# Performance work log

Hardware: AMD Instinct MI355X
Metric: run time of the kernel (lower is better)

## Reference

```python
import jax, jax.numpy as jnp
import numpy as np

B, E, S, D = 32, 64, 50, 300   # batch, sentences/essay, words/sentence, word dim
F = 100                        # conv filters (cnn_lstm_convunits_size)
H = 100                        # lstm units (cnn_lstm_att_pool_size)
W_WIN = 5                      # word window length


def setup_inputs() -> dict:
    key = jax.random.key(0)
    ks = jax.random.split(key, 12)
    n = lambda k, shape: (jax.random.normal(k, shape, jnp.float32) * 0.05)
    return {
        "essays": jax.random.normal(ks[0], (B, E, S, D), jnp.float32),
        "conv_k": n(ks[1], (1, W_WIN, D, F)),      # HWIO
        "conv_b": jnp.zeros((F,), jnp.float32),
        "att1_mat": n(ks[2], (F, F)),
        "att1_bias": n(ks[3], (F,)),
        "att1_vec": n(ks[4], (F, 1)),
        "lstm_W": n(ks[5], (F + H, 4 * H)),        # TF BasicLSTMCell kernel, gate order i,j,f,o
        "lstm_b": jnp.zeros((4 * H,), jnp.float32),
        "att2_mat": n(ks[6], (H, H)),
        "att2_bias": n(ks[7], (H,)),
        "att2_vec": n(ks[8], (H, 1)),
        "dense_w": n(ks[9], (H, 1)),
        "dense_b": jnp.zeros((1,), jnp.float32),
    }


def reference(essays, conv_k, conv_b, att1_mat, att1_bias, att1_vec,
              lstm_W, lstm_b, att2_mat, att2_bias, att2_vec,
              dense_w, dense_b):
    # conv2d, kernel [1, w_window_len], SAME padding, relu  -> [B,E,S,F]
    conv1 = jax.lax.conv_general_dilated(
        essays, conv_k, window_strides=(1, 1), padding="SAME",
        dimension_numbers=("NHWC", "HWIO", "NHWC"))
    conv1 = jax.nn.relu(conv1 + conv_b)

    # attention pooling over words (axis=2)
    a1 = jnp.tanh(jnp.einsum("besf,fg->besg", conv1, att1_mat) + att1_bias)
    a1 = jnp.einsum("besg,go->beso", a1, att1_vec)          # [B,E,S,1]
    a1 = jax.nn.softmax(a1, axis=2)
    sent = jnp.sum(a1 * conv1, axis=2)                       # [B,E,F]

    # BasicLSTMCell (forget_bias=1.0, gate order i,j,f,o) over sentence axis
    hdim = lstm_b.shape[0] // 4
    bsz = essays.shape[0]

    def step(carry, xt):
        c, h = carry
        z = jnp.concatenate([xt, h], axis=1) @ lstm_W + lstm_b
        i, j, f, o = jnp.split(z, 4, axis=1)
        c = c * jax.nn.sigmoid(f + 1.0) + jax.nn.sigmoid(i) * jnp.tanh(j)
        h = jax.nn.sigmoid(o) * jnp.tanh(c)
        return (c, h), h

    init = (jnp.zeros((bsz, hdim), sent.dtype), jnp.zeros((bsz, hdim), sent.dtype))
    xs = jnp.swapaxes(sent, 0, 1)                            # [E,B,F]
    _, hs = jax.lax.scan(step, init, xs)
    lstm = jnp.swapaxes(hs, 0, 1)                            # [B,E,H]

    # attention pooling over sentences (axis=1)
    a2 = jnp.tanh(jnp.einsum("beh,hg->beg", lstm, att2_mat) + att2_bias)
    a2 = jnp.einsum("beg,go->beo", a2, att2_vec)             # [B,E,1]
    a2 = jax.nn.softmax(a2, axis=1)
    essay_repr = jnp.sum(a2 * lstm, axis=1)                  # [B,H]

    preds = jax.nn.sigmoid(essay_repr @ dense_w + dense_b).reshape(-1)  # [B]
    return preds
```

## Files before the change

### kernel.cpp

```cpp
#include <hip/hip_runtime.h>
#include <hip/hip_bf16.h>
#include <stdint.h>

#define Bsz 32
#define Esz 64
#define Ssz 50
#define Dsz 300
#define Fsz 100
#define Hsz 100
#define WWIN 5

#define PX   328
#define PC   136
#define KT_CONV 50
#define NTILES  7
#define MTILES  4
#define NGRP 2214

typedef __attribute__((ext_vector_type(8))) short bf16x8;
typedef __attribute__((ext_vector_type(8))) unsigned short u16x8;
typedef __attribute__((ext_vector_type(4))) float f32x4;

__device__ __forceinline__ float sigmoid_fast(float x) {
    return 1.0f / (1.0f + __expf(-x));
}
__device__ __forceinline__ float tanhf_fast(float x) {
    const float ax = fabsf(x);
    const float e = __expf(2.0f * ax);
    const float t = 1.0f - 2.0f / (e + 1.0f);
    return copysignf(t, x);
}

__device__ __forceinline__ unsigned short f2bf(float x) {
    union { __hip_bfloat16 h; unsigned short u; } cv;
    cv.h = __float2bfloat16(x);
    return cv.u;
}
__device__ __forceinline__ unsigned int f2bf2(float lo, float hi) {
    union { __hip_bfloat162 h2; unsigned int u; } cv;
    cv.h2 = __float22bfloat162_rn(make_float2(lo, hi));
    return cv.u;
}
__device__ __forceinline__ float bf2f(unsigned short b) {
    union { uint32_t u; float f; } v; v.u = ((uint32_t)b) << 16;
    return v.f;
}

#define N_BTGC (KT_CONV * 112 * 32)
#define N_BTGA (4 * 112 * 32)
#define N_BTGW (4 * 400 * 32)

__global__ __launch_bounds__(256) void prep_kernel(
    const float* __restrict__ conv_k, const float* __restrict__ att1_mat,
    const float* __restrict__ lstm_W,
    unsigned short* __restrict__ BtgC, unsigned short* __restrict__ BtgA,
    unsigned short* __restrict__ BtgW)
{
    const int total = N_BTGC + N_BTGA + N_BTGW;
    for (int i = blockIdx.x * 256 + threadIdx.x; i < total; i += gridDim.x * 256) {
        if (i < N_BTGC) {
            const int kt = i / (112 * 32);
            const int r  = i % (112 * 32);
            const int n  = r / 32;
            const int kk = r % 32;
            const int w  = kt / 10;
            const int d  = (kt % 10) * 32 + kk;
            float val = (d < Dsz && n < Fsz) ? conv_k[((size_t)w * Dsz + d) * Fsz + n] : 0.f;
            BtgC[i] = f2bf(val);
        } else if (i < N_BTGC + N_BTGA) {
            const int j  = i - N_BTGC;
            const int kt = j / (112 * 32);
            const int r  = j % (112 * 32);
            const int n  = r / 32;
            const int kk = r % 32;
            const int k  = kt * 32 + kk;
            float val = (k < Fsz && n < Fsz) ? att1_mat[(size_t)k * Fsz + n] : 0.f;
            BtgA[j] = f2bf(val);
        } else {
            const int j  = i - N_BTGC - N_BTGA;
            const int kt = j / (400 * 32);
            const int r  = j % (400 * 32);
            const int n  = r / 32;
            const int kk = r % 32;
            const int k  = kt * 32 + kk;
            float val = (k < Fsz) ? lstm_W[(size_t)k * 400 + n] : 0.f;
            BtgW[j] = f2bf(val);
        }
    }
}

template<int G>
__device__ __forceinline__ void conv_loadB(
    const unsigned short* __restrict__ BtgC, int boff0, int boff1, bool has1,
    bf16x8 (&bR)[5][2])
{
#pragma unroll
    for (int i = 0; i < 5; ++i) {
        const int kt = G * 5 + i;
        bR[i][0] = *reinterpret_cast<const bf16x8*>(BtgC + kt * 3584 + boff0);
        bR[i][1] = has1 ? *reinterpret_cast<const bf16x8*>(BtgC + kt * 3584 + boff1)
                        : (bf16x8)0;
    }
}

template<int KT>
__device__ __forceinline__ void conv_loadA(
    const unsigned short* b0p, const unsigned short* b1p,
    const int (&abase)[MTILES], bf16x8 (&a)[2][MTILES])
{
    constexpr int w   = KT / 10;
    constexpr int t   = KT % 10;
    constexpr int off = w * PX + t * 32;
#pragma unroll
    for (int mt = 0; mt < MTILES; ++mt) {
        a[0][mt] = *reinterpret_cast<const bf16x8*>(&b0p[abase[mt] + off]);
        a[1][mt] = *reinterpret_cast<const bf16x8*>(&b1p[abase[mt] + off]);
    }
}

__device__ __forceinline__ void mfma16(
    const bf16x8 (&a)[2][MTILES], const bf16x8 (&b)[2], bool has1,
    f32x4 (&acc)[2][MTILES][2])
{
    __builtin_amdgcn_s_setprio(1);
#pragma unroll
    for (int es = 0; es < 2; ++es) {
#pragma unroll
        for (int mt = 0; mt < MTILES; ++mt) {
            acc[es][mt][0] = __builtin_amdgcn_mfma_f32_16x16x32_bf16(a[es][mt], b[0], acc[es][mt][0], 0, 0, 0);
            if (has1)
                acc[es][mt][1] = __builtin_amdgcn_mfma_f32_16x16x32_bf16(a[es][mt], b[1], acc[es][mt][1], 0, 0, 0);
        }
    }
    __builtin_amdgcn_s_setprio(0);
}

template<int KT>
__device__ __forceinline__ void conv_kt(
    const unsigned short* b0p, const unsigned short* b1p,
    const int (&abase)[MTILES], bool has1, const bf16x8 (&b)[2],
    bf16x8 (&aX)[2][MTILES], bf16x8 (&aY)[2][MTILES],
    f32x4 (&acc)[2][MTILES][2])
{
    constexpr bool even = (KT % 2) == 0;
    if constexpr (KT + 1 < KT_CONV) {
        if constexpr (even) conv_loadA<KT + 1>(b0p, b1p, abase, aY);
        else                conv_loadA<KT + 1>(b0p, b1p, abase, aX);
    }
    if constexpr (even) mfma16(aX, b, has1, acc);
    else                mfma16(aY, b, has1, acc);
}

template<int G>
__device__ __forceinline__ void conv_group(
    const unsigned short* b0p, const unsigned short* b1p,
    const int (&abase)[MTILES], bool has1, const bf16x8 (&bR)[5][2],
    bf16x8 (&aX)[2][MTILES], bf16x8 (&aY)[2][MTILES],
    f32x4 (&acc)[2][MTILES][2])
{
    conv_kt<G * 5 + 0>(b0p, b1p, abase, has1, bR[0], aX, aY, acc);
    conv_kt<G * 5 + 1>(b0p, b1p, abase, has1, bR[1], aX, aY, acc);
    conv_kt<G * 5 + 2>(b0p, b1p, abase, has1, bR[2], aX, aY, acc);
    conv_kt<G * 5 + 3>(b0p, b1p, abase, has1, bR[3], aX, aY, acc);
    conv_kt<G * 5 + 4>(b0p, b1p, abase, has1, bR[4], aX, aY, acc);
}

template<int KT>
__device__ __forceinline__ void att_loadA(
    const unsigned short* b0p, const unsigned short* b1p,
    const int (&abase2)[MTILES], bf16x8 (&a)[2][MTILES])
{
    constexpr int off = KT * 32;
#pragma unroll
    for (int mt = 0; mt < MTILES; ++mt) {
        a[0][mt] = *reinterpret_cast<const bf16x8*>(&b0p[abase2[mt] + off]);
        a[1][mt] = *reinterpret_cast<const bf16x8*>(&b1p[abase2[mt] + off]);
    }
}

__global__ __launch_bounds__(256, 2) void conv_att1_kernel(
    const float* __restrict__ essays,
    const unsigned short* __restrict__ BtgC,
    const unsigned short* __restrict__ BtgA,
    const float* __restrict__ conv_b,
    const float* __restrict__ att1_bias,
    const float* __restrict__ att1_vec,
    unsigned short* __restrict__ sent_bf)
{
    __shared__ __align__(16) unsigned short buf[2][54 * PX];
    __shared__ float u_s[2][64];
    __shared__ float alpha_s[2][64];

    const int be0 = blockIdx.x * 2;
    const int tid = threadIdx.x;
    const int lane = tid & 63;
    const int wid  = tid >> 6;
    const int ln   = lane & 15;
    const int qd   = lane >> 4;

    if (tid < 128) u_s[tid >> 6][tid & 63] = 0.f;

    const int nt0 = wid;
    const int nt1 = wid + 4;
    const bool has1 = (nt1 < NTILES);
    const int boff0 = (nt0 * 16 + ln) * 32 + 8 * qd;
    const int boff1 = (nt1 * 16 + ln) * 32 + 8 * qd;

    int abase[MTILES];
#pragma unroll
    for (int mt = 0; mt < MTILES; ++mt) {
        const int m = mt * 16 + ln;
        abase[mt] = (m < Ssz ? m : Ssz - 1) * PX + 8 * qd;
    }

    bf16x8 bX[5][2], bY[5][2];
    conv_loadB<0>(BtgC, boff0, boff1, has1, bX);
    conv_loadB<1>(BtgC, boff0, boff1, has1, bY);

#pragma unroll
    for (int es = 0; es < 2; ++es) {
        const float* in_g = essays + (size_t)(be0 + es) * (Ssz * Dsz);
        float4 va[9], vb[9];
        int rr[9], cc[9];
        bool hv[9], fv[9], gv[9];
#pragma unroll
        for (int it = 0; it < 9; ++it) {
            const int g  = tid + it * 256;
            const int r  = g / 41;
            const int c8 = (g - r * 41) * 8;
            const int s  = r - 2;
            gv[it] = (g < NGRP);
            hv[it] = gv[it] && (s >= 0) && (s < Ssz) && (c8 < Dsz);
            fv[it] = hv[it] && (c8 + 8 <= Dsz);
            const float* base = in_g + (hv[it] ? (s * Dsz + c8) : 0);
            va[it] = *reinterpret_cast<const float4*>(base);
            vb[it] = *reinterpret_cast<const float4*>(fv[it] ? base + 4 : base);
            rr[it] = r; cc[it] = c8;
        }
#pragma unroll
        for (int it = 0; it < 9; ++it) {
            if (!gv[it]) continue;
            const float e0 = hv[it] ? va[it].x : 0.f;
            const float e1 = hv[it] ? va[it].y : 0.f;
            const float e2 = hv[it] ? va[it].z : 0.f;
            const float e3 = hv[it] ? va[it].w : 0.f;
            const float e4 = fv[it] ? vb[it].x : 0.f;
            const float e5 = fv[it] ? vb[it].y : 0.f;
            const float e6 = fv[it] ? vb[it].z : 0.f;
            const float e7 = fv[it] ? vb[it].w : 0.f;
            uint4 o;
            o.x = f2bf2(e0, e1);
            o.y = f2bf2(e2, e3);
            o.z = f2bf2(e4, e5);
            o.w = f2bf2(e6, e7);
            *reinterpret_cast<uint4*>(&buf[es][rr[it] * PX + cc[it]]) = o;
        }
    }
    __syncthreads();

    const unsigned short* b0p = buf[0];
    const unsigned short* b1p = buf[1];

    f32x4 acc[2][MTILES][2];
#pragma unroll
    for (int es = 0; es < 2; ++es)
#pragma unroll
        for (int mt = 0; mt < MTILES; ++mt) { acc[es][mt][0] = (f32x4)0.f; acc[es][mt][1] = (f32x4)0.f; }

    {
        bf16x8 aX[2][MTILES], aY[2][MTILES];
        conv_loadA<0>(b0p, b1p, abase, aX);
        conv_group<0>(b0p, b1p, abase, has1, bX, aX, aY, acc);
        conv_loadB<2>(BtgC, boff0, boff1, has1, bX);
        conv_group<1>(b0p, b1p, abase, has1, bY, aX, aY, acc);
        conv_loadB<3>(BtgC, boff0, boff1, has1, bY);
        conv_group<2>(b0p, b1p, abase, has1, bX, aX, aY, acc);
        conv_loadB<4>(BtgC, boff0, boff1, has1, bX);
        conv_group<3>(b0p, b1p, abase, has1, bY, aX, aY, acc);
        conv_loadB<5>(BtgC, boff0, boff1, has1, bY);
        conv_group<4>(b0p, b1p, abase, has1, bX, aX, aY, acc);
        conv_loadB<6>(BtgC, boff0, boff1, has1, bX);
        conv_group<5>(b0p, b1p, abase, has1, bY, aX, aY, acc);
        conv_loadB<7>(BtgC, boff0, boff1, has1, bY);
        conv_group<6>(b0p, b1p, abase, has1, bX, aX, aY, acc);
        conv_loadB<8>(BtgC, boff0, boff1, has1, bX);
        conv_group<7>(b0p, b1p, abase, has1, bY, aX, aY, acc);
        conv_loadB<9>(BtgC, boff0, boff1, has1, bY);
        conv_group<8>(b0p, b1p, abase, has1, bX, aX, aY, acc);
        conv_group<9>(b0p, b1p, abase, has1, bY, aX, aY, acc);
    }

    bf16x8 a1b[4][2];
#pragma unroll
    for (int kt = 0; kt < 4; ++kt) {
        a1b[kt][0] = *reinterpret_cast<const bf16x8*>(BtgA + kt * 3584 + boff0);
        a1b[kt][1] = has1 ? *reinterpret_cast<const bf16x8*>(BtgA + kt * 3584 + boff1)
                          : (bf16x8)0;
    }
    __syncthreads();

    {
        const float bias0 = conv_b[nt0 * 16 + ln];
        const int n_g1 = nt1 * 16 + ln;
        const bool g1ok = has1 && (n_g1 < Fsz);
        const float bias1 = g1ok ? conv_b[n_g1] : 0.f;
#pragma unroll
        for (int es = 0; es < 2; ++es) {
#pragma unroll
            for (int mt = 0; mt < MTILES; ++mt) {
#pragma unroll
                for (int j = 0; j < 4; ++j) {
                    const int m_row = mt * 16 + qd * 4 + j;
                    buf[es][m_row * PC + nt0 * 16 + ln] = f2bf(fmaxf(acc[es][mt][0][j] + bias0, 0.f));
                    if (g1ok)
                        buf[es][m_row * PC + n_g1] = f2bf(fmaxf(acc[es][mt][1][j] + bias1, 0.f));
                }
            }
        }
    }
    for (int idx = tid; idx < 2 * 64 * 2; idx += 256) {
        const int es = idx >> 7;
        const int r2 = idx & 127;
        const int row = r2 >> 1;
        const int c = 112 + (r2 & 1) * 8;
        *reinterpret_cast<u16x8*>(&buf[es][row * PC + c]) = (u16x8)0;
    }
    __syncthreads();

    f32x4 acc2[2][MTILES][2];
#pragma unroll
    for (int es = 0; es < 2; ++es)
#pragma unroll
        for (int mt = 0; mt < MTILES; ++mt) { acc2[es][mt][0] = (f32x4)0.f; acc2[es][mt][1] = (f32x4)0.f; }

    {
        int abase2[MTILES];
#pragma unroll
        for (int mt = 0; mt < MTILES; ++mt) abase2[mt] = (mt * 16 + ln) * PC + 8 * qd;

        bf16x8 aX[2][MTILES], aY[2][MTILES];
        att_loadA<0>(b0p, b1p, abase2, aX);
        att_loadA<1>(b0p, b1p, abase2, aY);
        mfma16(aX, a1b[0], has1, acc2);
        att_loadA<2>(b0p, b1p, abase2, aX);
        mfma16(aY, a1b[1], has1, acc2);
        att_loadA<3>(b0p, b1p, abase2, aY);
        mfma16(aX, a1b[2], has1, acc2);
        mfma16(aY, a1b[3], has1, acc2);
    }

    {
        const int g0 = nt0 * 16 + ln;
        const float b1v0 = att1_bias[g0];
        const float vv0  = att1_vec[g0];
        const int g1 = nt1 * 16 + ln;
        const bool g1v = has1 && (g1 < Fsz);
        const float b1v1 = g1v ? att1_bias[g1] : 0.f;
        const float vv1  = g1v ? att1_vec[g1]  : 0.f;
#pragma unroll
        for (int es = 0; es < 2; ++es) {
#pragma unroll
            for (int mt = 0; mt < MTILES; ++mt) {
#pragma unroll
                for (int j = 0; j < 4; ++j) {
                    const int m_row = mt * 16 + qd * 4 + j;
                    float val = 0.f;
                    if (m_row < Ssz) {
                        val = tanhf_fast(acc2[es][mt][0][j] + b1v0) * vv0;
                        if (g1v) val += tanhf_fast(acc2[es][mt][1][j] + b1v1) * vv1;
                    }
                    val += __shfl_xor(val, 1);
                    val += __shfl_xor(val, 2);
                    val += __shfl_xor(val, 4);
                    val += __shfl_xor(val, 8);
                    if (ln == 0 && m_row < Ssz) atomicAdd(&u_s[es][m_row], val);
                }
            }
        }
    }
    __syncthreads();

    if (wid < 2) {
        const float uv = (lane < Ssz) ? u_s[wid][lane] : -1e30f;
        float m = uv;
#pragma unroll
        for (int off = 32; off > 0; off >>= 1) m = fmaxf(m, __shfl_xor(m, off));
        float e = (lane < Ssz) ? __expf(uv - m) : 0.f;
        float sum = e;
#pragma unroll
        for (int off = 32; off > 0; off >>= 1) sum += __shfl_xor(sum, off);
        alpha_s[wid][lane] = e / sum;
    }
    __syncthreads();

    {
        const int es = tid >> 7;
        const int f  = tid & 127;
        unsigned short v = 0;
        if (f < Fsz) {
            float a = 0.f;
            for (int s = 0; s < Ssz; ++s) a += alpha_s[es][s] * bf2f(buf[es][s * PC + f]);
            v = f2bf(a);
        }
        sent_bf[(size_t)(be0 + es) * 128 + f] = v;
    }
}

__global__ __launch_bounds__(256) void xpart_kernel(
    const unsigned short* __restrict__ sent_bf,
    const unsigned short* __restrict__ BtgW,
    const float* __restrict__ lstm_b,
    float* __restrict__ xpart)
{
    const int wid  = threadIdx.x >> 6;
    const int mt   = blockIdx.x * 4 + wid;
    const int lane = threadIdx.x & 63;
    const int ln   = lane & 15;
    const int qd   = lane >> 4;
    const int m0   = mt * 16;

    f32x4 acc[25];
#pragma unroll
    for (int nt = 0; nt < 25; ++nt) acc[nt] = (f32x4)0.f;

#pragma unroll
    for (int kt = 0; kt < 4; ++kt) {
        const bf16x8 a = *reinterpret_cast<const bf16x8*>(
            sent_bf + (size_t)(m0 + ln) * 128 + kt * 32 + 8 * qd);
#pragma unroll
        for (int nt = 0; nt < 25; ++nt) {
            const bf16x8 b = *reinterpret_cast<const bf16x8*>(
                BtgW + ((size_t)kt * 400 + nt * 16 + ln) * 32 + 8 * qd);
            acc[nt] = __builtin_amdgcn_mfma_f32_16x16x32_bf16(a, b, acc[nt], 0, 0, 0);
        }
    }

#pragma unroll
    for (int nt = 0; nt < 25; ++nt) {
        const int col = nt * 16 + ln;
        const float bias = lstm_b[col];
#pragma unroll
        for (int j = 0; j < 4; ++j) {
            const int row = m0 + qd * 4 + j;
            xpart[(size_t)row * 400 + col] = acc[nt][j] + bias;
        }
    }
}

__global__ __launch_bounds__(448) void lstm_att2_kernel(
    const float* __restrict__ xpart,
    const float* __restrict__ lstm_W,
    const float* __restrict__ att2_mat,
    const float* __restrict__ att2_bias,
    const float* __restrict__ att2_vec,
    const float* __restrict__ dense_w,
    const float* __restrict__ dense_b,
    float* __restrict__ out)
{
    __shared__ __align__(16) float h_s[Hsz];
    __shared__ float z_s[400];
    __shared__ __align__(16) float hist[Esz][Hsz];
    __shared__ float w2_s[Esz * Hsz];
    __shared__ float u2_s[Esz];
    __shared__ float alpha2_s[Esz];
    __shared__ float repr_s[Hsz];

    const int b = blockIdx.x;
    const int tid = threadIdx.x;
    const bool actv = tid < 400;

    float w[100];
    if (actv) {
#pragma unroll
        for (int k = 0; k < 100; ++k) w[k] = lstm_W[(size_t)(Fsz + k) * 400 + tid];
    }
    float c = 0.f;
    if (tid < Hsz) h_s[tid] = 0.f;
    __syncthreads();

    float xp_cur = actv ? xpart[(size_t)b * Esz * 400 + tid] : 0.f;
    const float4* h4 = reinterpret_cast<const float4*>(h_s);

    for (int t = 0; t < Esz; ++t) {
        const float xp_next = (actv && (t + 1) < Esz)
            ? xpart[((size_t)b * Esz + t + 1) * 400 + tid] : 0.f;
        if (actv) {
            float z0 = xp_cur, z1 = 0.f, z2 = 0.f, z3 = 0.f;
#pragma unroll
            for (int k4 = 0; k4 < 25; ++k4) {
                const float4 hv = h4[k4];
                z0 += hv.x * w[4 * k4 + 0];
                z1 += hv.y * w[4 * k4 + 1];
                z2 += hv.z * w[4 * k4 + 2];
                z3 += hv.w * w[4 * k4 + 3];
            }
            z_s[tid] = (z0 + z1) + (z2 + z3);
        }
        __syncthreads();

        if (tid < Hsz) {
            const float zi = z_s[tid];
            const float zj = z_s[tid + 100];
            const float zf = z_s[tid + 200];
            const float zo = z_s[tid + 300];
            c = c * sigmoid_fast(zf + 1.0f) + sigmoid_fast(zi) * tanhf_fast(zj);
            const float h = sigmoid_fast(zo) * tanhf_fast(c);
            h_s[tid] = h;
            hist[t][tid] = h;
        }
        __syncthreads();
        xp_cur = xp_next;
    }

    for (int idx = tid; idx < Esz * Hsz; idx += 448) {
        const int e = idx / Hsz;
        const int g = idx - e * Hsz;
        const float* lp = hist[e];
        float a0 = 0.f, a1 = 0.f, a2 = 0.f, a3 = 0.f;
        for (int k = 0; k < Hsz; k += 4) {
            a0 += lp[k + 0] * att2_mat[(k + 0) * Hsz + g];
            a1 += lp[k + 1] * att2_mat[(k + 1) * Hsz + g];
            a2 += lp[k + 2] * att2_mat[(k + 2) * Hsz + g];
            a3 += lp[k + 3] * att2_mat[(k + 3) * Hsz + g];
        }
        w2_s[idx] = tanhf_fast(att2_bias[g] + ((a0 + a1) + (a2 + a3))) * att2_vec[g];
    }
    __syncthreads();

    if (tid < Esz) {
        float acc = 0.f;
        const float* wp = w2_s + tid * Hsz;
        for (int g = 0; g < Hsz; ++g) acc += wp[g];
        u2_s[tid] = acc;
    }
    __syncthreads();

    if (tid < 64) {
        const float uv = u2_s[tid];
        float m = uv;
#pragma unroll
        for (int off = 32; off > 0; off >>= 1) m = fmaxf(m, __shfl_xor(m, off));
        float e = __expf(uv - m);
        float sum = e;
#pragma unroll
        for (int off = 32; off > 0; off >>= 1) sum += __shfl_xor(sum, off);
        alpha2_s[tid] = e / sum;
    }
    __syncthreads();

    if (tid < Hsz) {
        float acc = 0.f;
        for (int e = 0; e < Esz; ++e) acc += alpha2_s[e] * hist[e][tid];
        repr_s[tid] = acc;
    }
    __syncthreads();

    if (tid == 0) {
        float acc = dense_b[0];
        for (int hh = 0; hh < Hsz; ++hh) acc += repr_s[hh] * dense_w[hh];
        out[b] = sigmoid_fast(acc);
    }
}

extern "C" void kernel_launch(void* const* d_in, const int* in_sizes, int n_in,
                              void* d_out, int out_size, void* d_ws, size_t ws_size,
                              hipStream_t stream) {
    const float* essays    = (const float*)d_in[0];
    const float* conv_k    = (const float*)d_in[1];
    const float* conv_b    = (const float*)d_in[2];
    const float* att1_mat  = (const float*)d_in[3];
    const float* att1_bias = (const float*)d_in[4];
    const float* att1_vec  = (const float*)d_in[5];
    const float* lstm_W    = (const float*)d_in[6];
    const float* lstm_b    = (const float*)d_in[7];
    const float* att2_mat  = (const float*)d_in[8];
    const float* att2_bias = (const float*)d_in[9];
    const float* att2_vec  = (const float*)d_in[10];
    const float* dense_w   = (const float*)d_in[11];
    const float* dense_b   = (const float*)d_in[12];

    float* out = (float*)d_out;

    char* ws = (char*)d_ws;
    unsigned short* sent_bf = (unsigned short*)ws;
    float* xpart = (float*)(ws + 524288);
    unsigned short* BtgC = (unsigned short*)(ws + 3801088);
    unsigned short* BtgA = (unsigned short*)(ws + 4159488);
    unsigned short* BtgW = (unsigned short*)(ws + 4188160);

    prep_kernel<<<512, 256, 0, stream>>>(conv_k, att1_mat, lstm_W, BtgC, BtgA, BtgW);
    conv_att1_kernel<<<Bsz * Esz / 2, 256, 0, stream>>>(
        essays, BtgC, BtgA, conv_b, att1_bias, att1_vec, sent_bf);
    xpart_kernel<<<32, 256, 0, stream>>>(sent_bf, BtgW, lstm_b, xpart);
    lstm_att2_kernel<<<Bsz, 448, 0, stream>>>(
        xpart, lstm_W, att2_mat, att2_bias, att2_vec, dense_w, dense_b, out);
}
```

Baseline: 202.8 us.

## Batch LSTM recurrence across 16 essays per block using bf16 MFMA

Replaces the per-essay scalar LSTM loop (one block per essay, fp32 FMAs from registers) with a kernel that processes 16 essays per block. The hidden-to-gate product runs as bf16 MFMA, using gate-interleaved weights prepared in the prep kernel and hidden state double-buffered in swizzled LDS. The attention pooling is split into a separate kernel that reads the stored hidden history from global memory. The recurrence now runs on only 2 blocks with reduced-precision hidden state and needs an extra launch and global round-trip, in exchange for fewer serial FMA steps per timestep.

New measurement: 240.2 us. 1.18x slower.

```diff
diff --git a/kernel.cpp b/kernel.cpp
--- a/kernel.cpp
+++ b/kernel.cpp
@@ -49,14 +49,15 @@
 #define N_BTGC (KT_CONV * 112 * 32)
 #define N_BTGA (4 * 112 * 32)
 #define N_BTGW (4 * 400 * 32)
+#define N_BTGH (4 * 400 * 32)
 
 __global__ __launch_bounds__(256) void prep_kernel(
     const float* __restrict__ conv_k, const float* __restrict__ att1_mat,
     const float* __restrict__ lstm_W,
     unsigned short* __restrict__ BtgC, unsigned short* __restrict__ BtgA,
-    unsigned short* __restrict__ BtgW)
-{
-    const int total = N_BTGC + N_BTGA + N_BTGW;
+    unsigned short* __restrict__ BtgW, unsigned short* __restrict__ BtgH)
+{
+    const int total = N_BTGC + N_BTGA + N_BTGW + N_BTGH;
     for (int i = blockIdx.x * 256 + threadIdx.x; i < total; i += gridDim.x * 256) {
         if (i < N_BTGC) {
             const int kt = i / (112 * 32);
@@ -76,7 +77,7 @@
             const int k  = kt * 32 + kk;
             float val = (k < Fsz && n < Fsz) ? att1_mat[(size_t)k * Fsz + n] : 0.f;
             BtgA[j] = f2bf(val);
-        } else {
+        } else if (i < N_BTGC + N_BTGA + N_BTGW) {
             const int j  = i - N_BTGC - N_BTGA;
             const int kt = j / (400 * 32);
             const int r  = j % (400 * 32);
@@ -85,6 +86,17 @@
             const int k  = kt * 32 + kk;
             float val = (k < Fsz) ? lstm_W[(size_t)k * 400 + n] : 0.f;
             BtgW[j] = f2bf(val);
+        } else {
+            const int j  = i - N_BTGC - N_BTGA - N_BTGW;
+            const int kt = j / (400 * 32);
+            const int r  = j % (400 * 32);
+            const int gi = r / 32;
+            const int kk = r % 32;
+            const int k  = kt * 32 + kk;
+            const int gate = gi & 3;
+            const int cell = gi >> 2;
+            float val = (k < Hsz) ? lstm_W[(size_t)(Fsz + k) * 400 + gate * 100 + cell] : 0.f;
+            BtgH[j] = f2bf(val);
         }
     }
 }
@@ -410,7 +422,7 @@
     const unsigned short* __restrict__ sent_bf,
     const unsigned short* __restrict__ BtgW,
     const float* __restrict__ lstm_b,
-    float* __restrict__ xpart)
+    float* __restrict__ xpartT)
 {
     const int wid  = threadIdx.x >> 6;
     const int mt   = blockIdx.x * 4 + wid;
@@ -438,18 +450,121 @@
 #pragma unroll
     for (int nt = 0; nt < 25; ++nt) {
         const int col = nt * 16 + ln;
+        const int gate = col / 100;
+        const int cell = col - gate * 100;
         const float bias = lstm_b[col];
+        const int gi = cell * 4 + gate;
 #pragma unroll
         for (int j = 0; j < 4; ++j) {
             const int row = m0 + qd * 4 + j;
-            xpart[(size_t)row * 400 + col] = acc[nt][j] + bias;
-        }
-    }
-}
-
-__global__ __launch_bounds__(448) void lstm_att2_kernel(
-    const float* __restrict__ xpart,
-    const float* __restrict__ lstm_W,
+            const int b = row >> 6;
+            const int t = row & 63;
+            xpartT[((size_t)t * 32 + b) * 400 + gi] = acc[nt][j] + bias;
+        }
+    }
+}
+
+__global__ __launch_bounds__(512) void lstm_kernel(
+    const float* __restrict__ xpartT,
+    const unsigned short* __restrict__ BtgH,
+    float* __restrict__ hist)
+{
+    __shared__ __align__(16) unsigned short Hb[2][16 * 128];
+
+    const int tid  = threadIdx.x;
+    const int lane = tid & 63;
+    const int wid  = tid >> 6;
+    const int ln   = lane & 15;
+    const int qd   = lane >> 4;
+    const int bglob = blockIdx.x * 16 + ln;
+
+    const int mtbase = (wid * 25) >> 3;
+    const int cnt    = (((wid + 1) * 25) >> 3) - mtbase;
+
+    int mts[4];
+#pragma unroll
+    for (int s = 0; s < 4; ++s) mts[s] = mtbase + (s < cnt ? s : cnt - 1);
+
+    bf16x8 aW[4][4];
+#pragma unroll
+    for (int s = 0; s < 4; ++s)
+#pragma unroll
+        for (int kt = 0; kt < 4; ++kt)
+            aW[s][kt] = *reinterpret_cast<const bf16x8*>(
+                BtgH + ((size_t)kt * 400 + mts[s] * 16 + ln) * 32 + qd * 8);
+
+    *reinterpret_cast<uint4*>(reinterpret_cast<char*>(&Hb[0][0]) + tid * 16) =
+        make_uint4(0, 0, 0, 0);
+
+    int rdoff[4];
+#pragma unroll
+    for (int kt = 0; kt < 4; ++kt)
+        rdoff[kt] = ln * 256 + ((kt * 64 + qd * 16) ^ ((ln & 7) << 4));
+    int wroff[4];
+#pragma unroll
+    for (int s = 0; s < 4; ++s) {
+        const int cell = mts[s] * 4 + qd;
+        wroff[s] = ln * 256 + ((cell * 2) ^ ((ln & 7) << 4));
+    }
+
+    f32x4 acc[4];
+#pragma unroll
+    for (int s = 0; s < 4; ++s)
+        acc[s] = *reinterpret_cast<const f32x4*>(
+            xpartT + ((size_t)bglob) * 400 + mts[s] * 16 + qd * 4);
+
+    float c[4];
+#pragma unroll
+    for (int s = 0; s < 4; ++s) c[s] = 0.f;
+
+    char* HbBase = reinterpret_cast<char*>(&Hb[0][0]);
+    __syncthreads();
+
+    for (int t = 0; t < Esz; ++t) {
+        const char* curH = HbBase + (t & 1) * 4096;
+        char*       nxtH = HbBase + ((t + 1) & 1) * 4096;
+
+        bf16x8 bH[4];
+#pragma unroll
+        for (int kt = 0; kt < 4; ++kt)
+            bH[kt] = *reinterpret_cast<const bf16x8*>(curH + rdoff[kt]);
+
+        const int tn = (t + 1 < Esz) ? t + 1 : t;
+        f32x4 xp[4];
+#pragma unroll
+        for (int s = 0; s < 4; ++s)
+            xp[s] = *reinterpret_cast<const f32x4*>(
+                xpartT + ((size_t)tn * 32 + bglob) * 400 + mts[s] * 16 + qd * 4);
+
+        __builtin_amdgcn_s_setprio(1);
+#pragma unroll
+        for (int kt = 0; kt < 4; ++kt)
+#pragma unroll
+            for (int s = 0; s < 4; ++s)
+                acc[s] = __builtin_amdgcn_mfma_f32_16x16x32_bf16(aW[s][kt], bH[kt], acc[s], 0, 0, 0);
+        __builtin_amdgcn_s_setprio(0);
+
+#pragma unroll
+        for (int s = 0; s < 4; ++s) {
+            const float zi = acc[s][0], zj = acc[s][1], zf = acc[s][2], zo = acc[s][3];
+            c[s] = c[s] * sigmoid_fast(zf + 1.0f) + sigmoid_fast(zi) * tanhf_fast(zj);
+            const float h = sigmoid_fast(zo) * tanhf_fast(c[s]);
+            if (s < cnt) {
+                *reinterpret_cast<unsigned short*>(nxtH + wroff[s]) = f2bf(h);
+                const int cell = mts[s] * 4 + qd;
+                hist[((size_t)bglob * Esz + t) * Hsz + cell] = h;
+            }
+        }
+
+        __syncthreads();
+
+#pragma unroll
+        for (int s = 0; s < 4; ++s) acc[s] = xp[s];
+    }
+}
+
+__global__ __launch_bounds__(256) void att2_kernel(
+    const float* __restrict__ lstm,
     const float* __restrict__ att2_mat,
     const float* __restrict__ att2_bias,
     const float* __restrict__ att2_vec,
@@ -457,65 +572,22 @@
     const float* __restrict__ dense_b,
     float* __restrict__ out)
 {
-    __shared__ __align__(16) float h_s[Hsz];
-    __shared__ float z_s[400];
-    __shared__ __align__(16) float hist[Esz][Hsz];
+    __shared__ float l_s[Esz * Hsz];
     __shared__ float w2_s[Esz * Hsz];
     __shared__ float u2_s[Esz];
-    __shared__ float alpha2_s[Esz];
+    __shared__ float alpha_s[Esz];
     __shared__ float repr_s[Hsz];
 
     const int b = blockIdx.x;
     const int tid = threadIdx.x;
-    const bool actv = tid < 400;
-
-    float w[100];
-    if (actv) {
-#pragma unroll
-        for (int k = 0; k < 100; ++k) w[k] = lstm_W[(size_t)(Fsz + k) * 400 + tid];
-    }
-    float c = 0.f;
-    if (tid < Hsz) h_s[tid] = 0.f;
-    __syncthreads();
-
-    float xp_cur = actv ? xpart[(size_t)b * Esz * 400 + tid] : 0.f;
-    const float4* h4 = reinterpret_cast<const float4*>(h_s);
-
-    for (int t = 0; t < Esz; ++t) {
-        const float xp_next = (actv && (t + 1) < Esz)
-            ? xpart[((size_t)b * Esz + t + 1) * 400 + tid] : 0.f;
-        if (actv) {
-            float z0 = xp_cur, z1 = 0.f, z2 = 0.f, z3 = 0.f;
-#pragma unroll
-            for (int k4 = 0; k4 < 25; ++k4) {
-                const float4 hv = h4[k4];
-                z0 += hv.x * w[4 * k4 + 0];
-                z1 += hv.y * w[4 * k4 + 1];
-                z2 += hv.z * w[4 * k4 + 2];
-                z3 += hv.w * w[4 * k4 + 3];
-            }
-            z_s[tid] = (z0 + z1) + (z2 + z3);
-        }
-        __syncthreads();
-
-        if (tid < Hsz) {
-            const float zi = z_s[tid];
-            const float zj = z_s[tid + 100];
-            const float zf = z_s[tid + 200];
-            const float zo = z_s[tid + 300];
-            c = c * sigmoid_fast(zf + 1.0f) + sigmoid_fast(zi) * tanhf_fast(zj);
-            const float h = sigmoid_fast(zo) * tanhf_fast(c);
-            h_s[tid] = h;
-            hist[t][tid] = h;
-        }
-        __syncthreads();
-        xp_cur = xp_next;
-    }
-
-    for (int idx = tid; idx < Esz * Hsz; idx += 448) {
+
+    for (int i = tid; i < Esz * Hsz; i += 256) l_s[i] = lstm[(size_t)b * Esz * Hsz + i];
+    __syncthreads();
+
+    for (int idx = tid; idx < Esz * Hsz; idx += 256) {
         const int e = idx / Hsz;
         const int g = idx - e * Hsz;
-        const float* lp = hist[e];
+        const float* lp = l_s + e * Hsz;
         float a0 = 0.f, a1 = 0.f, a2 = 0.f, a3 = 0.f;
         for (int k = 0; k < Hsz; k += 4) {
             a0 += lp[k + 0] * att2_mat[(k + 0) * Hsz + g];
@@ -527,11 +599,11 @@
     }
     __syncthreads();
 
-    if (tid < Esz) {
+    for (int e = tid; e < Esz; e += 256) {
         float acc = 0.f;
-        const float* wp = w2_s + tid * Hsz;
+        const float* wp = w2_s + e * Hsz;
         for (int g = 0; g < Hsz; ++g) acc += wp[g];
-        u2_s[tid] = acc;
+        u2_s[e] = acc;
     }
     __syncthreads();
 
@@ -544,14 +616,14 @@
         float sum = e;
 #pragma unroll
         for (int off = 32; off > 0; off >>= 1) sum += __shfl_xor(sum, off);
-        alpha2_s[tid] = e / sum;
-    }
-    __syncthreads();
-
-    if (tid < Hsz) {
+        alpha_s[tid] = e / sum;
+    }
+    __syncthreads();
+
+    for (int hh = tid; hh < Hsz; hh += 256) {
         float acc = 0.f;
-        for (int e = 0; e < Esz; ++e) acc += alpha2_s[e] * hist[e][tid];
-        repr_s[tid] = acc;
+        for (int e = 0; e < Esz; ++e) acc += alpha_s[e] * l_s[e * Hsz + hh];
+        repr_s[hh] = acc;
     }
     __syncthreads();
 
@@ -583,15 +655,18 @@
 
     char* ws = (char*)d_ws;
     unsigned short* sent_bf = (unsigned short*)ws;
-    float* xpart = (float*)(ws + 524288);
-    unsigned short* BtgC = (unsigned short*)(ws + 3801088);
-    unsigned short* BtgA = (unsigned short*)(ws + 4159488);
-    unsigned short* BtgW = (unsigned short*)(ws + 4188160);
-
-    prep_kernel<<<512, 256, 0, stream>>>(conv_k, att1_mat, lstm_W, BtgC, BtgA, BtgW);
+    float* xpartT = (float*)(ws + 524288);
+    float* hist   = (float*)(ws + 3801088);
+    unsigned short* BtgC = (unsigned short*)(ws + 4620288);
+    unsigned short* BtgA = (unsigned short*)(ws + 4978688);
+    unsigned short* BtgW = (unsigned short*)(ws + 5007360);
+    unsigned short* BtgH = (unsigned short*)(ws + 5109760);
+
+    prep_kernel<<<512, 256, 0, stream>>>(conv_k, att1_mat, lstm_W, BtgC, BtgA, BtgW, BtgH);
     conv_att1_kernel<<<Bsz * Esz / 2, 256, 0, stream>>>(
         essays, BtgC, BtgA, conv_b, att1_bias, att1_vec, sent_bf);
-    xpart_kernel<<<32, 256, 0, stream>>>(sent_bf, BtgW, lstm_b, xpart);
-    lstm_att2_kernel<<<Bsz, 448, 0, stream>>>(
-        xpart, lstm_W, att2_mat, att2_bias, att2_vec, dense_w, dense_b, out);
-}
+    xpart_kernel<<<32, 256, 0, stream>>>(sent_bf, BtgW, lstm_b, xpartT);
+    lstm_kernel<<<2, 512, 0, stream>>>(xpartT, BtgH, hist);
+    att2_kernel<<<Bsz, 256, 0, stream>>>(
+        hist, att2_mat, att2_bias, att2_vec, dense_w, dense_b, out);
+}
```

## Interleave LSTM gates per cell and use shuffles to halve per-step barriers

Applied to the files above, without the earlier changes.

The xpart GEMM now writes its output with the four gate values of each cell stored next to each other. Each LSTM thread therefore owns one gate of one cell, and the four gates are combined with wave shuffles instead of a shared-memory round trip followed by a barrier. A double-buffered h vector removes one __syncthreads per timestep. The whole per-essay xpart slab is also preloaded into LDS up front, which takes the global load off the recurrence path at the cost of about 100KB of LDS, reused afterwards for the attention scratch.

Result: slower. 207.9 us (+2.5%).

```diff
diff --git a/kernel.cpp b/kernel.cpp
--- a/kernel.cpp
+++ b/kernel.cpp
@@ -410,7 +410,7 @@
     const unsigned short* __restrict__ sent_bf,
     const unsigned short* __restrict__ BtgW,
     const float* __restrict__ lstm_b,
-    float* __restrict__ xpart)
+    float* __restrict__ xpartB)
 {
     const int wid  = threadIdx.x >> 6;
     const int mt   = blockIdx.x * 4 + wid;
@@ -438,17 +438,20 @@
 #pragma unroll
     for (int nt = 0; nt < 25; ++nt) {
         const int col = nt * 16 + ln;
+        const int gate = col / 100;
+        const int cell = col - gate * 100;
         const float bias = lstm_b[col];
+        const int gi = cell * 4 + gate;
 #pragma unroll
         for (int j = 0; j < 4; ++j) {
             const int row = m0 + qd * 4 + j;
-            xpart[(size_t)row * 400 + col] = acc[nt][j] + bias;
+            xpartB[(size_t)row * 400 + gi] = acc[nt][j] + bias;
         }
     }
 }
 
 __global__ __launch_bounds__(448) void lstm_att2_kernel(
-    const float* __restrict__ xpart,
+    const float* __restrict__ xpartB,
     const float* __restrict__ lstm_W,
     const float* __restrict__ att2_mat,
     const float* __restrict__ att2_bias,
@@ -457,35 +460,42 @@
     const float* __restrict__ dense_b,
     float* __restrict__ out)
 {
-    __shared__ __align__(16) float h_s[Hsz];
-    __shared__ float z_s[400];
-    __shared__ __align__(16) float hist[Esz][Hsz];
-    __shared__ float w2_s[Esz * Hsz];
+    __shared__ __align__(16) float xp_lds[Esz * 400];
+    __shared__ __align__(16) float hist[Esz * Hsz];
+    __shared__ __align__(16) float h_lds[2][Hsz];
     __shared__ float u2_s[Esz];
     __shared__ float alpha2_s[Esz];
     __shared__ float repr_s[Hsz];
 
-    const int b = blockIdx.x;
+    const int b   = blockIdx.x;
     const int tid = threadIdx.x;
+    const int lane = tid & 63;
     const bool actv = tid < 400;
+    const int cell = tid >> 2;
+    const int g    = tid & 3;
+    const int qbase = lane & 60;
+
+    {
+        const float4* src = reinterpret_cast<const float4*>(xpartB + (size_t)b * Esz * 400);
+        float4* dst = reinterpret_cast<float4*>(xp_lds);
+        for (int i = tid; i < Esz * 100; i += 448) dst[i] = src[i];
+    }
 
     float w[100];
     if (actv) {
-#pragma unroll
-        for (int k = 0; k < 100; ++k) w[k] = lstm_W[(size_t)(Fsz + k) * 400 + tid];
-    }
+        const int col = g * 100 + cell;
+#pragma unroll
+        for (int k = 0; k < 100; ++k) w[k] = lstm_W[(size_t)(Fsz + k) * 400 + col];
+    }
+    if (tid < Hsz) h_lds[0][tid] = 0.f;
     float c = 0.f;
-    if (tid < Hsz) h_s[tid] = 0.f;
-    __syncthreads();
-
-    float xp_cur = actv ? xpart[(size_t)b * Esz * 400 + tid] : 0.f;
-    const float4* h4 = reinterpret_cast<const float4*>(h_s);
+    __syncthreads();
 
     for (int t = 0; t < Esz; ++t) {
-        const float xp_next = (actv && (t + 1) < Esz)
-            ? xpart[((size_t)b * Esz + t + 1) * 400 + tid] : 0.f;
+        float z = 0.f;
         if (actv) {
-            float z0 = xp_cur, z1 = 0.f, z2 = 0.f, z3 = 0.f;
+            const float4* h4 = reinterpret_cast<const float4*>(h_lds[t & 1]);
+            float z0 = xp_lds[t * 400 + tid], z1 = 0.f, z2 = 0.f, z3 = 0.f;
 #pragma unroll
             for (int k4 = 0; k4 < 25; ++k4) {
                 const float4 hv = h4[k4];
@@ -494,43 +504,43 @@
                 z2 += hv.z * w[4 * k4 + 2];
                 z3 += hv.w * w[4 * k4 + 3];
             }
-            z_s[tid] = (z0 + z1) + (z2 + z3);
-        }
-        __syncthreads();
-
-        if (tid < Hsz) {
-            const float zi = z_s[tid];
-            const float zj = z_s[tid + 100];
-            const float zf = z_s[tid + 200];
-            const float zo = z_s[tid + 300];
+            z = (z0 + z1) + (z2 + z3);
+        }
+        const float zi = __shfl(z, qbase + 0);
+        const float zj = __shfl(z, qbase + 1);
+        const float zf = __shfl(z, qbase + 2);
+        const float zo = __shfl(z, qbase + 3);
+        if (actv) {
             c = c * sigmoid_fast(zf + 1.0f) + sigmoid_fast(zi) * tanhf_fast(zj);
             const float h = sigmoid_fast(zo) * tanhf_fast(c);
-            h_s[tid] = h;
-            hist[t][tid] = h;
+            if (g == 0) {
+                h_lds[(t + 1) & 1][cell] = h;
+                hist[t * Hsz + cell] = h;
+            }
         }
         __syncthreads();
-        xp_cur = xp_next;
-    }
-
+    }
+
+    float* w2_s = xp_lds;
     for (int idx = tid; idx < Esz * Hsz; idx += 448) {
         const int e = idx / Hsz;
-        const int g = idx - e * Hsz;
-        const float* lp = hist[e];
+        const int gg = idx - e * Hsz;
+        const float* lp = hist + e * Hsz;
         float a0 = 0.f, a1 = 0.f, a2 = 0.f, a3 = 0.f;
         for (int k = 0; k < Hsz; k += 4) {
-            a0 += lp[k + 0] * att2_mat[(k + 0) * Hsz + g];
-            a1 += lp[k + 1] * att2_mat[(k + 1) * Hsz + g];
-            a2 += lp[k + 2] * att2_mat[(k + 2) * Hsz + g];
-            a3 += lp[k + 3] * att2_mat[(k + 3) * Hsz + g];
-        }
-        w2_s[idx] = tanhf_fast(att2_bias[g] + ((a0 + a1) + (a2 + a3))) * att2_vec[g];
+            a0 += lp[k + 0] * att2_mat[(k + 0) * Hsz + gg];
+            a1 += lp[k + 1] * att2_mat[(k + 1) * Hsz + gg];
+            a2 += lp[k + 2] * att2_mat[(k + 2) * Hsz + gg];
+            a3 += lp[k + 3] * att2_mat[(k + 3) * Hsz + gg];
+        }
+        w2_s[idx] = tanhf_fast(att2_bias[gg] + ((a0 + a1) + (a2 + a3))) * att2_vec[gg];
     }
     __syncthreads();
 
     if (tid < Esz) {
         float acc = 0.f;
         const float* wp = w2_s + tid * Hsz;
-        for (int g = 0; g < Hsz; ++g) acc += wp[g];
+        for (int gg = 0; gg < Hsz; ++gg) acc += wp[gg];
         u2_s[tid] = acc;
     }
     __syncthreads();
@@ -550,7 +560,7 @@
 
     if (tid < Hsz) {
         float acc = 0.f;
-        for (int e = 0; e < Esz; ++e) acc += alpha2_s[e] * hist[e][tid];
+        for (int e = 0; e < Esz; ++e) acc += alpha2_s[e] * hist[e * Hsz + tid];
         repr_s[tid] = acc;
     }
     __syncthreads();
@@ -583,7 +593,7 @@
 
     char* ws = (char*)d_ws;
     unsigned short* sent_bf = (unsigned short*)ws;
-    float* xpart = (float*)(ws + 524288);
+    float* xpartB = (float*)(ws + 524288);
     unsigned short* BtgC = (unsigned short*)(ws + 3801088);
     unsigned short* BtgA = (unsigned short*)(ws + 4159488);
     unsigned short* BtgW = (unsigned short*)(ws + 4188160);
@@ -591,7 +601,7 @@
     prep_kernel<<<512, 256, 0, stream>>>(conv_k, att1_mat, lstm_W, BtgC, BtgA, BtgW);
     conv_att1_kernel<<<Bsz * Esz / 2, 256, 0, stream>>>(
         essays, BtgC, BtgA, conv_b, att1_bias, att1_vec, sent_bf);
-    xpart_kernel<<<32, 256, 0, stream>>>(sent_bf, BtgW, lstm_b, xpart);
+    xpart_kernel<<<32, 256, 0, stream>>>(sent_bf, BtgW, lstm_b, xpartB);
     lstm_att2_kernel<<<Bsz, 448, 0, stream>>>(
-        xpart, lstm_W, att2_mat, att2_bias, att2_vec, dense_w, dense_b, out);
-}
+        xpartB, lstm_W, att2_mat, att2_bias, att2_vec, dense_w, dense_b, out);
+}
```
